# Kernel tuning notes

Hardware: AMD Instinct MI355X
Metric: run time of the kernel (lower is better)

Reference implementation:

```python
import jax, jax.numpy as jnp
import numpy as np

F = 200      # number of independent feature MLPs
D_IN = 3
H = 15       # enc_out // 2
ENC = 30     # enc_out
B = 32768


def setup_inputs() -> dict:
    key = jax.random.key(0)
    ky, k1, kb1, k2, kb2, k3, kb3 = jax.random.split(key, 7)
    y = jax.random.normal(ky, (B, F, D_IN), dtype=jnp.float32)
    # Per-feature MLP params, stacked along feature axis (grouped GEMM form).
    W1 = jax.random.normal(k1, (F, D_IN, H), dtype=jnp.float32) * (1.0 / np.sqrt(D_IN))
    b1 = jax.random.normal(kb1, (F, H), dtype=jnp.float32) * 0.01
    W2 = jax.random.normal(k2, (F, H, ENC), dtype=jnp.float32) * (1.0 / np.sqrt(H))
    b2 = jax.random.normal(kb2, (F, ENC), dtype=jnp.float32) * 0.01
    # Final linear over the concatenated [F*ENC] vector.
    W3 = jax.random.normal(k3, (F * ENC, 1), dtype=jnp.float32) * (1.0 / np.sqrt(F * ENC))
    b3 = jax.random.normal(kb3, (1,), dtype=jnp.float32) * 0.01
    return {"y": y, "W1": W1, "b1": b1, "W2": W2, "b2": b2, "W3": W3, "b3": b3}


def reference(y, W1, b1, W2, b2, W3, b3):
    # 200 independent tiny MLPs -> one batched einsum per layer.
    h = jax.nn.relu(jnp.einsum('bfi,fih->bfh', y, W1) + b1)      # [B, F, H]
    h = jax.nn.relu(jnp.einsum('bfh,fhe->bfe', h, W2) + b2)      # [B, F, ENC]
    # torch.cat(res, 1) with res[i] = block_i(y[:, i, :]) == reshape [B, F*ENC]
    flat = h.reshape(h.shape[0], F * ENC)
    return flat @ W3 + b3                                         # [B, 1]
```

## Files before the change

### kernel.cpp

```cpp
#include <hip/hip_runtime.h>
#include <hip/hip_bf16.h>

#define NF  200
#define DIN 3
#define NH  15
#define NE  30
#define NB  32768

typedef __attribute__((ext_vector_type(8)))  short short8;
typedef __attribute__((ext_vector_type(16))) float f32x16;

constexpr int FSPLIT = 25;
constexpr int FPW    = NF / FSPLIT;
constexpr int PAIRS  = FPW / 2;
constexpr int NBATCH = FPW / 4;
constexpr int BT     = 256;
constexpr int RPW    = 32;
constexpr int RPB    = 4 * RPW;

constexpr size_t OFF_A1P = 0;
constexpr size_t OFF_W2Q = 102400;
constexpr size_t OFF_W3F = 307200;

__device__ __forceinline__ unsigned f2bfu(float x) {
    __hip_bfloat16 h = __float2bfloat16(x);
    unsigned short u; __builtin_memcpy(&u, &h, 2); return (unsigned)u;
}

__device__ __forceinline__ unsigned cvtpk(float lo, float hi) {
    unsigned r;
    asm("v_cvt_pk_bf16_f32 %0, %1, %2" : "=v"(r) : "v"(lo), "v"(hi));
    return r;
}

__global__ void nn_init(float* __restrict__ out, const float* __restrict__ b3) {
    int i = blockIdx.x * 256 + threadIdx.x;
    if (i < NB) out[i] = b3[0];
}

__global__ void nn_prep(const float* __restrict__ W1, const float* __restrict__ b1,
                        const float* __restrict__ W2, const float* __restrict__ b2,
                        const float* __restrict__ W3, char* __restrict__ ws) {
    const int f = blockIdx.x;
    const int t = threadIdx.x;
    const int x = t & 31, hi = t >> 5;
    unsigned short* A1p = (unsigned short*)(ws + OFF_A1P);
    unsigned short* W2q = (unsigned short*)(ws + OFF_W2Q);
    float*          w3f = (float*)(ws + OFF_W3F);

    {
        unsigned short* d = W2q + ((size_t)f * 64 + t) * 8;
#pragma unroll
        for (int j = 0; j < 8; ++j) {
            const int h = (j & 3) + 8 * (j >> 2) + 4 * hi;
            float v = 0.f;
            if (x < NE) v = (h < NH) ? W2[((size_t)f * NH + h) * NE + x]
                                     : b2[f * NE + x];
            d[j] = (unsigned short)f2bfu(v);
        }
    }
    if (t < 32) {
        const int hh = t >> 4, r = t & 15;
        const int e = (r & 3) + 8 * (r >> 2) + 4 * hh;
        w3f[(size_t)f * 32 + t] = (e < NE) ? W3[f * NE + e] : 0.f;
    }

    if ((f & 1) == 0) {
        unsigned short* a = A1p + ((size_t)(f >> 1) * 64 + t) * 8;
#pragma unroll
        for (int j = 0; j < 8; ++j) {
            float v = 0.f;
            if (hi == 0) {
                if (x < 16) {
                    if (x < NH) {
                        if (j < 3)       v = W1[((size_t)f * DIN + j) * NH + x];
                        else if (j == 3) v = b1[f * NH + x];
                    }
                } else {
                    const int h = x - 16;
                    if (h < NH) {
                        if (j >= 4 && j < 7) v = W1[((size_t)(f + 1) * DIN + (j - 4)) * NH + h];
                        else if (j == 7)     v = b1[(f + 1) * NH + h];
                    }
                }
            }
            a[j] = (unsigned short)f2bfu(v);
        }
    }
}

__global__ __launch_bounds__(BT, 5)
void nn_main(const float* __restrict__ y, const char* __restrict__ ws,
             float* __restrict__ out) {
    __shared__ __align__(16) short sA1[PAIRS * 512];
    __shared__ __align__(16) short sW2[FPW * 512];
    __shared__ __align__(16) float sW3f[FPW * 32];

    const int t  = threadIdx.x;
    const int w  = t >> 6;
    const int l  = t & 63;
    const int ln = l & 31;
    const int hi = l >> 5;
    const int r0 = blockIdx.x * RPB + w * RPW;
    const int f0 = blockIdx.y * FPW;
    const int p0 = f0 >> 1;

    {
        const uint4* gA = (const uint4*)(ws + OFF_A1P + (size_t)p0 * 1024);
        const uint4* gW = (const uint4*)(ws + OFF_W2Q + (size_t)f0 * 1024);
        const uint4* g3 = (const uint4*)(ws + OFF_W3F + (size_t)f0 * 128);
        uint4* dA = (uint4*)sA1;
        uint4* dW = (uint4*)sW2;
        uint4* d3 = (uint4*)sW3f;
        dA[t] = gA[t];
        dW[t]       = gW[t];
        dW[t + 256] = gW[t + 256];
        if (t < 64) d3[t] = g3[t];
    }
    __syncthreads();

    const float4* __restrict__ yp4 = reinterpret_cast<const float4*>(
        y + (size_t)(r0 + ln) * (NF * DIN) + (size_t)f0 * DIN);
    const short* __restrict__ a1l = sA1 + l * 8;
    const short* __restrict__ w2l = sW2 + l * 8;

    const unsigned himask = hi ? 0x3F800000u : 0u;
    const float onef = 1.0f;
    const f32x16 zc = {};

    float partial = 0.f;

    auto pair_body = [&](int pp, float y0A, float y1A, float y2A,
                                 float y0B, float y1B, float y2B) {
        const short8 A1  = *reinterpret_cast<const short8*>(a1l + (size_t)pp * 512);
        const short8 W2A = *reinterpret_cast<const short8*>(w2l + (size_t)(2 * pp) * 512);
        const short8 W2B = *reinterpret_cast<const short8*>(w2l + (size_t)(2 * pp + 1) * 512);

        union { unsigned u[4]; short8 s; } B1;
        B1.u[0] = cvtpk(y0A, y1A);
        B1.u[1] = cvtpk(y2A, onef);
        B1.u[2] = cvtpk(y0B, y1B);
        B1.u[3] = cvtpk(y2B, onef);

        const f32x16 d1 = __builtin_amdgcn_mfma_f32_32x32x16_bf16(A1, B1.s, zc, 0, 0, 0);

        union { unsigned u[4]; short8 s; } PA, PB;
#pragma unroll
        for (int i = 0; i < 4; ++i) {
            PA.u[i] = cvtpk(fmaxf(d1[2 * i], 0.f),     fmaxf(d1[2 * i + 1], 0.f));
            PB.u[i] = cvtpk(fmaxf(d1[8 + 2 * i], 0.f), fmaxf(d1[8 + 2 * i + 1], 0.f));
        }
        PA.u[3] |= himask;
        PB.u[3] |= himask;

        {
            const f32x16 dA2 = __builtin_amdgcn_mfma_f32_32x32x16_bf16(W2A, PA.s, zc, 0, 0, 0);
            const float4* wf = (const float4*)(sW3f + (2 * pp) * 32 + hi * 16);
            const float4 w0 = wf[0], w1 = wf[1];
            partial = fmaf(fmaxf(dA2[0], 0.f), w0.x, partial);
            partial = fmaf(fmaxf(dA2[1], 0.f), w0.y, partial);
            partial = fmaf(fmaxf(dA2[2], 0.f), w0.z, partial);
            partial = fmaf(fmaxf(dA2[3], 0.f), w0.w, partial);
            partial = fmaf(fmaxf(dA2[4], 0.f), w1.x, partial);
            partial = fmaf(fmaxf(dA2[5], 0.f), w1.y, partial);
            partial = fmaf(fmaxf(dA2[6], 0.f), w1.z, partial);
            partial = fmaf(fmaxf(dA2[7], 0.f), w1.w, partial);
            const float4 w2_ = wf[2], w3_ = wf[3];
            partial = fmaf(fmaxf(dA2[8],  0.f), w2_.x, partial);
            partial = fmaf(fmaxf(dA2[9],  0.f), w2_.y, partial);
            partial = fmaf(fmaxf(dA2[10], 0.f), w2_.z, partial);
            partial = fmaf(fmaxf(dA2[11], 0.f), w2_.w, partial);
            partial = fmaf(fmaxf(dA2[12], 0.f), w3_.x, partial);
            partial = fmaf(fmaxf(dA2[13], 0.f), w3_.y, partial);
            partial = fmaf(fmaxf(dA2[14], 0.f), w3_.z, partial);
            partial = fmaf(fmaxf(dA2[15], 0.f), w3_.w, partial);
        }
        {
            const f32x16 dB2 = __builtin_amdgcn_mfma_f32_32x32x16_bf16(W2B, PB.s, zc, 0, 0, 0);
            const float4* wf = (const float4*)(sW3f + (2 * pp + 1) * 32 + hi * 16);
            const float4 w0 = wf[0], w1 = wf[1];
            partial = fmaf(fmaxf(dB2[0], 0.f), w0.x, partial);
            partial = fmaf(fmaxf(dB2[1], 0.f), w0.y, partial);
            partial = fmaf(fmaxf(dB2[2], 0.f), w0.z, partial);
            partial = fmaf(fmaxf(dB2[3], 0.f), w0.w, partial);
            partial = fmaf(fmaxf(dB2[4], 0.f), w1.x, partial);
            partial = fmaf(fmaxf(dB2[5], 0.f), w1.y, partial);
            partial = fmaf(fmaxf(dB2[6], 0.f), w1.z, partial);
            partial = fmaf(fmaxf(dB2[7], 0.f), w1.w, partial);
            const float4 w2_ = wf[2], w3_ = wf[3];
            partial = fmaf(fmaxf(dB2[8],  0.f), w2_.x, partial);
            partial = fmaf(fmaxf(dB2[9],  0.f), w2_.y, partial);
            partial = fmaf(fmaxf(dB2[10], 0.f), w2_.z, partial);
            partial = fmaf(fmaxf(dB2[11], 0.f), w2_.w, partial);
            partial = fmaf(fmaxf(dB2[12], 0.f), w3_.x, partial);
            partial = fmaf(fmaxf(dB2[13], 0.f), w3_.y, partial);
            partial = fmaf(fmaxf(dB2[14], 0.f), w3_.z, partial);
            partial = fmaf(fmaxf(dB2[15], 0.f), w3_.w, partial);
        }
    };

#pragma unroll 1
    for (int bi = 0; bi < NBATCH; ++bi) {
        const float4 c0 = yp4[3 * bi + 0];
        const float4 c1 = yp4[3 * bi + 1];
        const float4 c2 = yp4[3 * bi + 2];
        pair_body(2 * bi,     c0.x, c0.y, c0.z,  c0.w, c1.x, c1.y);
        pair_body(2 * bi + 1, c1.z, c1.w, c2.x,  c2.y, c2.z, c2.w);
    }

    partial += __shfl_xor(partial, 32);
    if (hi == 0) atomicAdd(&out[r0 + ln], partial);
}

extern "C" void kernel_launch(void* const* d_in, const int* in_sizes, int n_in,
                              void* d_out, int out_size, void* d_ws, size_t ws_size,
                              hipStream_t stream) {
    const float* y  = (const float*)d_in[0];
    const float* W1 = (const float*)d_in[1];
    const float* b1 = (const float*)d_in[2];
    const float* W2 = (const float*)d_in[3];
    const float* b2 = (const float*)d_in[4];
    const float* W3 = (const float*)d_in[5];
    const float* b3 = (const float*)d_in[6];
    float* out = (float*)d_out;

    nn_prep<<<dim3(NF), dim3(64), 0, stream>>>(W1, b1, W2, b2, W3, (char*)d_ws);
    nn_init<<<dim3((NB + 255) / 256), dim3(256), 0, stream>>>(out, b3);
    nn_main<<<dim3(NB / RPB, FSPLIT), dim3(BT), 0, stream>>>(
        y, (const char*)d_ws, out);
}
```

Baseline: 42.63 us.

## Prefetch y before weight staging, fully unroll loop, use packed FMA epilogue

All six float4 loads of the y inputs are now issued before the shared-memory weight staging and barrier, so global latency overlaps the staging. The two-iteration loop is fully unrolled. The scalar FMA chain for the W3 dot product is replaced by v_pk_fma_f32 into two float2 accumulators, halving the FMA instruction count and breaking the serial dependency. The cost is more live registers under launch_bounds(256,5) and a different floating-point summation order.

```diff
diff --git a/kernel.cpp b/kernel.cpp
--- a/kernel.cpp
+++ b/kernel.cpp
@@ -13,7 +13,6 @@
 constexpr int FSPLIT = 25;
 constexpr int FPW    = NF / FSPLIT;
 constexpr int PAIRS  = FPW / 2;
-constexpr int NBATCH = FPW / 4;
 constexpr int BT     = 256;
 constexpr int RPW    = 32;
 constexpr int RPB    = 4 * RPW;
@@ -31,6 +30,12 @@
     unsigned r;
     asm("v_cvt_pk_bf16_f32 %0, %1, %2" : "=v"(r) : "v"(lo), "v"(hi));
     return r;
+}
+
+__device__ __forceinline__ float2 pkfma(float2 a, float2 b, float2 c) {
+    float2 d;
+    asm("v_pk_fma_f32 %0, %1, %2, %3" : "=v"(d) : "v"(a), "v"(b), "v"(c));
+    return d;
 }
 
 __global__ void nn_init(float* __restrict__ out, const float* __restrict__ b3) {
@@ -105,6 +110,11 @@
     const int f0 = blockIdx.y * FPW;
     const int p0 = f0 >> 1;
 
+    const float4* __restrict__ yp4 = reinterpret_cast<const float4*>(
+        y + (size_t)(r0 + ln) * (NF * DIN) + (size_t)f0 * DIN);
+    const float4 c0 = yp4[0], c1 = yp4[1], c2 = yp4[2];
+    const float4 c3 = yp4[3], c4 = yp4[4], c5 = yp4[5];
+
     {
         const uint4* gA = (const uint4*)(ws + OFF_A1P + (size_t)p0 * 1024);
         const uint4* gW = (const uint4*)(ws + OFF_W2Q + (size_t)f0 * 1024);
@@ -119,8 +129,6 @@
     }
     __syncthreads();
 
-    const float4* __restrict__ yp4 = reinterpret_cast<const float4*>(
-        y + (size_t)(r0 + ln) * (NF * DIN) + (size_t)f0 * DIN);
     const short* __restrict__ a1l = sA1 + l * 8;
     const short* __restrict__ w2l = sW2 + l * 8;
 
@@ -128,7 +136,26 @@
     const float onef = 1.0f;
     const f32x16 zc = {};
 
-    float partial = 0.f;
+    float2 acc0 = {0.f, 0.f};
+    float2 acc1 = {0.f, 0.f};
+
+    auto epilogue = [&](const f32x16& d2, const float* __restrict__ wf) {
+        float r[16];
+#pragma unroll
+        for (int i = 0; i < 16; ++i) r[i] = fmaxf(d2[i], 0.f);
+        const float4 w0  = ((const float4*)wf)[0];
+        const float4 w1  = ((const float4*)wf)[1];
+        const float4 w2_ = ((const float4*)wf)[2];
+        const float4 w3_ = ((const float4*)wf)[3];
+        acc0 = pkfma(float2{r[0],  r[1]},  float2{w0.x,  w0.y},  acc0);
+        acc1 = pkfma(float2{r[2],  r[3]},  float2{w0.z,  w0.w},  acc1);
+        acc0 = pkfma(float2{r[4],  r[5]},  float2{w1.x,  w1.y},  acc0);
+        acc1 = pkfma(float2{r[6],  r[7]},  float2{w1.z,  w1.w},  acc1);
+        acc0 = pkfma(float2{r[8],  r[9]},  float2{w2_.x, w2_.y}, acc0);
+        acc1 = pkfma(float2{r[10], r[11]}, float2{w2_.z, w2_.w}, acc1);
+        acc0 = pkfma(float2{r[12], r[13]}, float2{w3_.x, w3_.y}, acc0);
+        acc1 = pkfma(float2{r[14], r[15]}, float2{w3_.z, w3_.w}, acc1);
+    };
 
     auto pair_body = [&](int pp, float y0A, float y1A, float y2A,
                                  float y0B, float y1B, float y2B) {
@@ -153,61 +180,18 @@
         PA.u[3] |= himask;
         PB.u[3] |= himask;
 
-        {
-            const f32x16 dA2 = __builtin_amdgcn_mfma_f32_32x32x16_bf16(W2A, PA.s, zc, 0, 0, 0);
-            const float4* wf = (const float4*)(sW3f + (2 * pp) * 32 + hi * 16);
-            const float4 w0 = wf[0], w1 = wf[1];
-            partial = fmaf(fmaxf(dA2[0], 0.f), w0.x, partial);
-            partial = fmaf(fmaxf(dA2[1], 0.f), w0.y, partial);
-            partial = fmaf(fmaxf(dA2[2], 0.f), w0.z, partial);
-            partial = fmaf(fmaxf(dA2[3], 0.f), w0.w, partial);
-            partial = fmaf(fmaxf(dA2[4], 0.f), w1.x, partial);
-            partial = fmaf(fmaxf(dA2[5], 0.f), w1.y, partial);
-            partial = fmaf(fmaxf(dA2[6], 0.f), w1.z, partial);
-            partial = fmaf(fmaxf(dA2[7], 0.f), w1.w, partial);
-            const float4 w2_ = wf[2], w3_ = wf[3];
-            partial = fmaf(fmaxf(dA2[8],  0.f), w2_.x, partial);
-            partial = fmaf(fmaxf(dA2[9],  0.f), w2_.y, partial);
-            partial = fmaf(fmaxf(dA2[10], 0.f), w2_.z, partial);
-            partial = fmaf(fmaxf(dA2[11], 0.f), w2_.w, partial);
-            partial = fmaf(fmaxf(dA2[12], 0.f), w3_.x, partial);
-            partial = fmaf(fmaxf(dA2[13], 0.f), w3_.y, partial);
-            partial = fmaf(fmaxf(dA2[14], 0.f), w3_.z, partial);
-            partial = fmaf(fmaxf(dA2[15], 0.f), w3_.w, partial);
-        }
-        {
-            const f32x16 dB2 = __builtin_amdgcn_mfma_f32_32x32x16_bf16(W2B, PB.s, zc, 0, 0, 0);
-            const float4* wf = (const float4*)(sW3f + (2 * pp + 1) * 32 + hi * 16);
-            const float4 w0 = wf[0], w1 = wf[1];
-            partial = fmaf(fmaxf(dB2[0], 0.f), w0.x, partial);
-            partial = fmaf(fmaxf(dB2[1], 0.f), w0.y, partial);
-            partial = fmaf(fmaxf(dB2[2], 0.f), w0.z, partial);
-            partial = fmaf(fmaxf(dB2[3], 0.f), w0.w, partial);
-            partial = fmaf(fmaxf(dB2[4], 0.f), w1.x, partial);
-            partial = fmaf(fmaxf(dB2[5], 0.f), w1.y, partial);
-            partial = fmaf(fmaxf(dB2[6], 0.f), w1.z, partial);
-            partial = fmaf(fmaxf(dB2[7], 0.f), w1.w, partial);
-            const float4 w2_ = wf[2], w3_ = wf[3];
-            partial = fmaf(fmaxf(dB2[8],  0.f), w2_.x, partial);
-            partial = fmaf(fmaxf(dB2[9],  0.f), w2_.y, partial);
-            partial = fmaf(fmaxf(dB2[10], 0.f), w2_.z, partial);
-            partial = fmaf(fmaxf(dB2[11], 0.f), w2_.w, partial);
-            partial = fmaf(fmaxf(dB2[12], 0.f), w3_.x, partial);
-            partial = fmaf(fmaxf(dB2[13], 0.f), w3_.y, partial);
-            partial = fmaf(fmaxf(dB2[14], 0.f), w3_.z, partial);
-            partial = fmaf(fmaxf(dB2[15], 0.f), w3_.w, partial);
-        }
+        const f32x16 dA2 = __builtin_amdgcn_mfma_f32_32x32x16_bf16(W2A, PA.s, zc, 0, 0, 0);
+        epilogue(dA2, sW3f + (2 * pp) * 32 + hi * 16);
+        const f32x16 dB2 = __builtin_amdgcn_mfma_f32_32x32x16_bf16(W2B, PB.s, zc, 0, 0, 0);
+        epilogue(dB2, sW3f + (2 * pp + 1) * 32 + hi * 16);
     };
 
-#pragma unroll 1
-    for (int bi = 0; bi < NBATCH; ++bi) {
-        const float4 c0 = yp4[3 * bi + 0];
-        const float4 c1 = yp4[3 * bi + 1];
-        const float4 c2 = yp4[3 * bi + 2];
-        pair_body(2 * bi,     c0.x, c0.y, c0.z,  c0.w, c1.x, c1.y);
-        pair_body(2 * bi + 1, c1.z, c1.w, c2.x,  c2.y, c2.z, c2.w);
-    }
-
+    pair_body(0, c0.x, c0.y, c0.z,  c0.w, c1.x, c1.y);
+    pair_body(1, c1.z, c1.w, c2.x,  c2.y, c2.z, c2.w);
+    pair_body(2, c3.x, c3.y, c3.z,  c3.w, c4.x, c4.y);
+    pair_body(3, c4.z, c4.w, c5.x,  c5.y, c5.z, c5.w);
+
+    float partial = (acc0.x + acc1.x) + (acc0.y + acc1.y);
     partial += __shfl_xor(partial, 32);
     if (hi == 0) atomicAdd(&out[r0 + ln], partial);
 }
```

Result: no change. 42.61 us (-0.0%).
